# Optimization experiments

Measured on AMD Instinct MI355X. Metric: run time of the kernel, lower is better.

The kernel has to match this reference:

```python
import jax, jax.numpy as jnp
import numpy as np

NEG_SLOPE = 0.2   # PyG GATConv default leaky_relu slope
BN_EPS = 1e-5
SM_EPS = 1e-16    # PyG segment-softmax denominator epsilon


def gat_conv(x, src, dst, W, a_src, a_dst, bias, heads, out_ch, concat):
    # x: [N, F_in]; src/dst: [E] (self-loops already included)
    N = x.shape[0]
    h = (x @ W).reshape(N, heads, out_ch)              # [N, H, C]
    s = jnp.sum(h * a_src, axis=-1)                    # [N, H] per-node source score
    d = jnp.sum(h * a_dst, axis=-1)                    # [N, H] per-node dest score
    e = jax.nn.leaky_relu(s[src] + d[dst], NEG_SLOPE)  # [E, H]
    # segment softmax over edges grouped by destination node
    m = jax.ops.segment_max(e, dst, num_segments=N)
    m = jnp.where(jnp.isfinite(m), m, 0.0)
    p = jnp.exp(e - m[dst])                            # [E, H]
    denom = jax.ops.segment_sum(p, dst, num_segments=N)
    alpha = p / (denom[dst] + SM_EPS)                  # [E, H]
    # attention-weighted scatter-sum aggregation
    out = jax.ops.segment_sum(h[src] * alpha[:, :, None], dst, num_segments=N)  # [N, H, C]
    if concat:
        out = out.reshape(N, heads * out_ch)
    else:
        out = out.mean(axis=1)
    return out + bias


def setup_inputs() -> dict:
    key = jax.random.key(0)
    ks = jax.random.split(key, 12)
    N, E = 50000, 400000
    F_in, hidden, H1, H2, nclasses = 256, 64, 4, 1, 40
    x = jax.random.normal(ks[0], (N, F_in), dtype=jnp.float32)
    edge_index = jax.random.randint(ks[1], (2, E), 0, N, dtype=jnp.int64)
    g = 1.0 / np.sqrt(F_in)
    W1 = jax.random.normal(ks[2], (F_in, H1 * hidden), dtype=jnp.float32) * g
    a_src1 = jax.random.normal(ks[3], (H1, hidden), dtype=jnp.float32) * 0.1
    a_dst1 = jax.random.normal(ks[4], (H1, hidden), dtype=jnp.float32) * 0.1
    b1 = jnp.zeros((H1 * hidden,), dtype=jnp.float32)
    gamma = jnp.ones((H1 * hidden,), dtype=jnp.float32)
    beta = jnp.zeros((H1 * hidden,), dtype=jnp.float32)
    g2 = 1.0 / np.sqrt(H1 * hidden)
    W2 = jax.random.normal(ks[5], (H1 * hidden, H2 * nclasses), dtype=jnp.float32) * g2
    a_src2 = jax.random.normal(ks[6], (H2, nclasses), dtype=jnp.float32) * 0.1
    a_dst2 = jax.random.normal(ks[7], (H2, nclasses), dtype=jnp.float32) * 0.1
    b2 = jnp.zeros((nclasses,), dtype=jnp.float32)
    return {"x": x, "edge_index": edge_index, "W1": W1, "a_src1": a_src1,
            "a_dst1": a_dst1, "b1": b1, "gamma": gamma, "beta": beta,
            "W2": W2, "a_src2": a_src2, "a_dst2": a_dst2, "b2": b2}


def reference(x, edge_index, W1, a_src1, a_dst1, b1, gamma, beta, W2, a_src2, a_dst2, b2):
    N = x.shape[0]
    loop = jnp.arange(N, dtype=edge_index.dtype)
    src = jnp.concatenate([edge_index[0], loop])   # add self-loops (GATConv default)
    dst = jnp.concatenate([edge_index[1], loop])
    H1, hidden = a_src1.shape
    H2, nclasses = a_src2.shape
    h = gat_conv(x, src, dst, W1, a_src1, a_dst1, b1, H1, hidden, concat=True)
    # BatchNorm1d (training-mode batch statistics, biased variance)
    mu = h.mean(axis=0)
    var = h.var(axis=0)
    h = (h - mu) * jax.lax.rsqrt(var + BN_EPS) * gamma + beta
    h = jax.nn.elu(h)
    out = gat_conv(h, src, dst, W2, a_src2, a_dst2, b2, H2, nclasses, concat=False)
    return jax.nn.log_softmax(out, axis=-1)
```

## Files before the change

### kernel.cpp

```cpp
#include <hip/hip_runtime.h>
#include <hip/hip_fp16.h>

constexpr int FIN = 256;
constexpr int C1  = 256;
constexpr int HID = 64;
constexpr int H1N = 4;
constexpr int NC  = 40;
constexpr int CAP = 256;
constexpr int CAP2 = 128;

__global__ __launch_bounds__(64)
void detect_kernel(const int* __restrict__ ei, int* __restrict__ flag, int E)
{
    int lane = threadIdx.x;
    int q = lane * (E / 64);
    int v = ei[2 * q + 1];
    unsigned long long nz = __ballot(v != 0);
    if (lane == 0) flag[0] = (nz == 0ull) ? 2 : 1;
}

__global__ __launch_bounds__(256)
void init_kernel(int* __restrict__ counts, int* __restrict__ fill,
                 float* __restrict__ colsum, float* __restrict__ colsq, int N)
{
    int t = blockIdx.x * 256 + threadIdx.x;
    if (t < N) { counts[t] = 1; fill[t] = 0; }
    if (t < C1) { colsum[t] = 0.f; colsq[t] = 0.f; }
}

__global__ __launch_bounds__(256)
void gemm1_kernel(const float* __restrict__ X, const float* __restrict__ W,
                  const float* __restrict__ as1, const float* __restrict__ ad1,
                  __half* __restrict__ Hm, float* __restrict__ s1,
                  float* __restrict__ d1, int N)
{
    __shared__ float As[16][68];
    __shared__ float Bs[16][68];
    const int t    = threadIdx.x;
    const int tx   = t & 15;
    const int ty   = t >> 4;
    const int bm   = blockIdx.x * 64;
    const int head = blockIdx.y;
    const int bn   = head * 64;

    const int lrow = t >> 2;
    const int lk   = (t & 3) * 4;
    const int brow = t >> 4;
    const int bcol = (t & 15) * 4;

    float acc[4][4] = {};

    for (int k0 = 0; k0 < FIN; k0 += 16) {
        int ar = bm + lrow; if (ar > N - 1) ar = N - 1;
        float4 av = *(const float4*)(X + (size_t)ar * FIN + k0 + lk);
        float4 bv = *(const float4*)(W + (size_t)(k0 + brow) * C1 + bn + bcol);
        As[lk + 0][lrow] = av.x;
        As[lk + 1][lrow] = av.y;
        As[lk + 2][lrow] = av.z;
        As[lk + 3][lrow] = av.w;
        *(float4*)&Bs[brow][bcol] = bv;
        __syncthreads();
        #pragma unroll
        for (int kk = 0; kk < 16; ++kk) {
            float4 a = *(const float4*)&As[kk][ty * 4];
            float4 b = *(const float4*)&Bs[kk][tx * 4];
            float a4[4] = {a.x, a.y, a.z, a.w};
            float b4[4] = {b.x, b.y, b.z, b.w};
            #pragma unroll
            for (int i = 0; i < 4; ++i)
                #pragma unroll
                for (int j = 0; j < 4; ++j)
                    acc[i][j] += a4[i] * b4[j];
        }
        __syncthreads();
    }

    float sp[4] = {0, 0, 0, 0}, dp[4] = {0, 0, 0, 0};
    #pragma unroll
    for (int i = 0; i < 4; ++i) {
        int row = bm + ty * 4 + i;
        if (row < N) {
            __half2 p01 = __floats2half2_rn(acc[i][0], acc[i][1]);
            __half2 p23 = __floats2half2_rn(acc[i][2], acc[i][3]);
            uint2 pk;
            pk.x = *(unsigned int*)&p01;
            pk.y = *(unsigned int*)&p23;
            *(uint2*)(Hm + (size_t)row * C1 + bn + tx * 4) = pk;
            #pragma unroll
            for (int j = 0; j < 4; ++j) {
                int col = tx * 4 + j;
                float v = acc[i][j];
                sp[i] += v * as1[bn + col];
                dp[i] += v * ad1[bn + col];
            }
        }
    }
    #pragma unroll
    for (int off = 1; off < 16; off <<= 1) {
        #pragma unroll
        for (int i = 0; i < 4; ++i) {
            sp[i] += __shfl_xor(sp[i], off);
            dp[i] += __shfl_xor(dp[i], off);
        }
    }
    if (tx == 0) {
        #pragma unroll
        for (int i = 0; i < 4; ++i) {
            int row = bm + ty * 4 + i;
            if (row < N) {
                s1[row * H1N + head] = sp[i];
                d1[row * H1N + head] = dp[i];
            }
        }
    }
}

__global__ __launch_bounds__(256)
void hist_kernel(const int* __restrict__ ei, const int* __restrict__ flag,
                 int* __restrict__ counts, int E)
{
    int t = blockIdx.x * 256 + threadIdx.x;
    int stride = flag[0];
    if (t < E) atomicAdd(&counts[ei[(size_t)stride * (E + t)]], 1);
}

__global__ __launch_bounds__(1024)
void scan_kernel(const int* __restrict__ cnt, int* __restrict__ offs, int N)
{
    __shared__ int wsum[16];
    __shared__ int carry_s;
    const int t = threadIdx.x, lane = t & 63, w = t >> 6;
    if (t == 0) carry_s = 0;
    __syncthreads();
    for (int base = 0; base < N; base += 1024) {
        int idx = base + t;
        int v = (idx < N) ? cnt[idx] : 0;
        int incl = v;
        #pragma unroll
        for (int off = 1; off < 64; off <<= 1) {
            int u = __shfl_up(incl, off);
            if (lane >= off) incl += u;
        }
        if (lane == 63) wsum[w] = incl;
        __syncthreads();
        int wpre = 0;
        for (int i = 0; i < w; ++i) wpre += wsum[i];
        int c = carry_s;
        if (idx < N) offs[idx] = c + wpre + incl - v;
        __syncthreads();
        if (t == 1023) carry_s = c + wpre + incl;
        __syncthreads();
    }
    if (t == 0) offs[N] = carry_s;
}

__global__ __launch_bounds__(256)
void scatter_kernel(const int* __restrict__ ei, const int* __restrict__ flag,
                    const int* __restrict__ offs, int* __restrict__ fill,
                    int* __restrict__ ssrc, int E, int N)
{
    int t = blockIdx.x * 256 + threadIdx.x;
    if (t >= E + N) return;
    int stride = flag[0];
    int s, d;
    if (t < E) {
        s = ei[(size_t)stride * t];
        d = ei[(size_t)stride * (E + t)];
    } else {
        s = t - E; d = s;
    }
    int pos = offs[d] + atomicAdd(&fill[d], 1);
    ssrc[pos] = s;
}

__global__ __launch_bounds__(256)
void agg1_kernel(const __half* __restrict__ Hm, const float* __restrict__ s1,
                 const float* __restrict__ d1, const int* __restrict__ offs,
                 const int* __restrict__ ssrc, const float* __restrict__ b1,
                 float* __restrict__ out1, int N)
{
    __shared__ float alpha[H1N][CAP];
    __shared__ int   srcs[CAP];
    __shared__ float invs[H1N];
    const int n    = blockIdx.x;
    const int t    = threadIdx.x;
    const int lane = t & 63;
    const int w    = t >> 6;
    const int beg  = offs[n], end = offs[n + 1];
    const int deg  = end - beg;
    const float dh = d1[n * H1N + w];

    if (deg <= CAP) {
        float mloc = -1e30f;
        for (int i = lane; i < deg; i += 64) {
            int s = ssrc[beg + i];
            if (w == 0) srcs[i] = s;
            float e = s1[s * H1N + w] + dh;
            e = e > 0.f ? e : 0.2f * e;
            alpha[w][i] = e;
            mloc = fmaxf(mloc, e);
        }
        #pragma unroll
        for (int off = 32; off; off >>= 1) mloc = fmaxf(mloc, __shfl_xor(mloc, off));
        float ssum = 0.f;
        for (int i = lane; i < deg; i += 64) {
            float ex = __expf(alpha[w][i] - mloc);
            alpha[w][i] = ex;
            ssum += ex;
        }
        #pragma unroll
        for (int off = 32; off; off >>= 1) ssum += __shfl_xor(ssum, off);
        if (lane == 0) invs[w] = 1.f / (ssum + 1e-16f);
        __syncthreads();

        float acc0 = 0.f, acc1 = 0.f, acc2 = 0.f, acc3 = 0.f;
        int i = 0;
        for (; i + 4 <= deg; i += 4) {
            int s0 = srcs[i],     s1i = srcs[i + 1];
            int s2 = srcs[i + 2], s3i = srcs[i + 3];
            float a0 = alpha[w][i],     a1 = alpha[w][i + 1];
            float a2 = alpha[w][i + 2], a3 = alpha[w][i + 3];
            float v0 = __half2float(Hm[(size_t)s0  * C1 + t]);
            float v1 = __half2float(Hm[(size_t)s1i * C1 + t]);
            float v2 = __half2float(Hm[(size_t)s2  * C1 + t]);
            float v3 = __half2float(Hm[(size_t)s3i * C1 + t]);
            acc0 += v0 * a0; acc1 += v1 * a1;
            acc2 += v2 * a2; acc3 += v3 * a3;
        }
        for (; i < deg; ++i)
            acc0 += __half2float(Hm[(size_t)srcs[i] * C1 + t]) * alpha[w][i];
        float acc = (acc0 + acc1) + (acc2 + acc3);
        out1[(size_t)n * C1 + t] = acc * invs[w] + b1[t];
        return;
    }

    float mloc = -1e30f;
    for (int p = beg + lane; p < end; p += 64) {
        float e = s1[ssrc[p] * H1N + w] + dh;
        e = e > 0.f ? e : 0.2f * e;
        mloc = fmaxf(mloc, e);
    }
    #pragma unroll
    for (int off = 32; off; off >>= 1) mloc = fmaxf(mloc, __shfl_xor(mloc, off));
    float ssum = 0.f;
    for (int p = beg + lane; p < end; p += 64) {
        float e = s1[ssrc[p] * H1N + w] + dh;
        e = e > 0.f ? e : 0.2f * e;
        ssum += __expf(e - mloc);
    }
    #pragma unroll
    for (int off = 32; off; off >>= 1) ssum += __shfl_xor(ssum, off);
    if (lane == 0) invs[w] = 1.f / (ssum + 1e-16f);

    float acc0 = 0.f, acc1 = 0.f, acc2 = 0.f, acc3 = 0.f;
    for (int c0 = 0; c0 < deg; c0 += CAP) {
        int cnt = min(CAP, deg - c0);
        for (int i = lane; i < cnt; i += 64) {
            int p = beg + c0 + i;
            int s = ssrc[p];
            if (w == 0) srcs[i] = s;
            float e = s1[s * H1N + w] + dh;
            e = e > 0.f ? e : 0.2f * e;
            alpha[w][i] = __expf(e - mloc);
        }
        __syncthreads();
        int i = 0;
        for (; i + 4 <= cnt; i += 4) {
            int s0 = srcs[i],     s1i = srcs[i + 1];
            int s2 = srcs[i + 2], s3i = srcs[i + 3];
            float a0 = alpha[w][i],     a1 = alpha[w][i + 1];
            float a2 = alpha[w][i + 2], a3 = alpha[w][i + 3];
            float v0 = __half2float(Hm[(size_t)s0  * C1 + t]);
            float v1 = __half2float(Hm[(size_t)s1i * C1 + t]);
            float v2 = __half2float(Hm[(size_t)s2  * C1 + t]);
            float v3 = __half2float(Hm[(size_t)s3i * C1 + t]);
            acc0 += v0 * a0; acc1 += v1 * a1;
            acc2 += v2 * a2; acc3 += v3 * a3;
        }
        for (; i < cnt; ++i)
            acc0 += __half2float(Hm[(size_t)srcs[i] * C1 + t]) * alpha[w][i];
        __syncthreads();
    }
    float acc = (acc0 + acc1) + (acc2 + acc3);
    out1[(size_t)n * C1 + t] = acc * invs[w] + b1[t];
}

__global__ __launch_bounds__(256)
void bnstats_kernel(const float* __restrict__ out1, float* __restrict__ colsum,
                    float* __restrict__ colsq, int N)
{
    int t = threadIdx.x;
    float s = 0.f, q = 0.f;
    for (int r = blockIdx.x; r < N; r += gridDim.x) {
        float v = out1[(size_t)r * C1 + t];
        s += v; q += v * v;
    }
    atomicAdd(&colsum[t], s);
    atomicAdd(&colsq[t], q);
}

__global__ __launch_bounds__(256)
void bnfin_kernel(const float* __restrict__ colsum, const float* __restrict__ colsq,
                  const float* __restrict__ gamma, const float* __restrict__ beta,
                  float* __restrict__ scale, float* __restrict__ shift, int N)
{
    int t = threadIdx.x;
    float mu  = colsum[t] / (float)N;
    float var = colsq[t] / (float)N - mu * mu;
    float sc  = gamma[t] * rsqrtf(var + 1e-5f);
    scale[t] = sc;
    shift[t] = beta[t] - mu * sc;
}

__global__ __launch_bounds__(256)
void gemm2_kernel(const float* __restrict__ out1, const float* __restrict__ scale,
                  const float* __restrict__ shift, const float* __restrict__ W2,
                  const float* __restrict__ as2, const float* __restrict__ ad2,
                  float* __restrict__ h2, float* __restrict__ s2,
                  float* __restrict__ d2, int N)
{
    __shared__ float Asm[64][68];
    __shared__ float Wsm[64 * 48];
    const int t   = threadIdx.x;
    const int r   = t >> 2;
    const int jg  = t & 3;
    const int rb  = blockIdx.x * 64;
    const int row = rb + r;
    const int j0  = jg * 10;

    float acc[10] = {};

    for (int kc = 0; kc < C1; kc += 64) {
        #pragma unroll
        for (int idx = t; idx < 64 * 16; idx += 256) {
            int ar = idx >> 4;
            int cg = (idx & 15) * 4;
            int arow = rb + ar;
            float4 v = make_float4(0.f, 0.f, 0.f, 0.f);
            if (arow < N) {
                v = *(const float4*)(out1 + (size_t)arow * C1 + kc + cg);
                float4 sc = *(const float4*)(scale + kc + cg);
                float4 sh = *(const float4*)(shift + kc + cg);
                v.x = v.x * sc.x + sh.x;
                v.y = v.y * sc.y + sh.y;
                v.z = v.z * sc.z + sh.z;
                v.w = v.w * sc.w + sh.w;
                v.x = v.x > 0.f ? v.x : (__expf(v.x) - 1.f);
                v.y = v.y > 0.f ? v.y : (__expf(v.y) - 1.f);
                v.z = v.z > 0.f ? v.z : (__expf(v.z) - 1.f);
                v.w = v.w > 0.f ? v.w : (__expf(v.w) - 1.f);
            }
            *(float4*)&Asm[ar][cg] = v;
        }
        #pragma unroll
        for (int idx = t; idx < 64 * 40; idx += 256) {
            int k = idx / 40, j = idx - k * 40;
            Wsm[k * 48 + (j / 10) * 12 + (j % 10)] = W2[(size_t)(kc + k) * NC + j];
        }
        __syncthreads();
        #pragma unroll 4
        for (int k = 0; k < 64; ++k) {
            float a = Asm[r][k];
            const float* wp = &Wsm[k * 48 + jg * 12];
            float4 w0 = *(const float4*)(wp);
            float4 w1 = *(const float4*)(wp + 4);
            float2 wv = *(const float2*)(wp + 8);
            acc[0] += a * w0.x; acc[1] += a * w0.y;
            acc[2] += a * w0.z; acc[3] += a * w0.w;
            acc[4] += a * w1.x; acc[5] += a * w1.y;
            acc[6] += a * w1.z; acc[7] += a * w1.w;
            acc[8] += a * wv.x; acc[9] += a * wv.y;
        }
        __syncthreads();
    }

    float sp = 0.f, dp = 0.f;
    #pragma unroll
    for (int jj = 0; jj < 10; ++jj) {
        sp += acc[jj] * as2[j0 + jj];
        dp += acc[jj] * ad2[j0 + jj];
    }
    sp += __shfl_xor(sp, 1); sp += __shfl_xor(sp, 2);
    dp += __shfl_xor(dp, 1); dp += __shfl_xor(dp, 2);
    if (row < N) {
        if (jg == 0) { s2[row] = sp; d2[row] = dp; }
        #pragma unroll
        for (int jj = 0; jj < 10; jj += 2)
            *(float2*)(h2 + (size_t)row * NC + j0 + jj) =
                make_float2(acc[jj], acc[jj + 1]);
    }
}

__global__ __launch_bounds__(256)
void agg2_kernel(const float* __restrict__ h2, const float* __restrict__ s2,
                 const float* __restrict__ d2, const int* __restrict__ offs,
                 const int* __restrict__ ssrc, const float* __restrict__ b2,
                 float* __restrict__ out, int N)
{
    __shared__ float al[4][CAP2];
    __shared__ int   sr[4][CAP2];
    int w = threadIdx.x >> 6;
    int node = blockIdx.x * 4 + w;
    if (node >= N) return;
    int lane = threadIdx.x & 63;
    int beg = offs[node], end = offs[node + 1];
    int deg = end - beg;
    float dn = d2[node];

    float v;
    if (deg <= CAP2) {
        float mloc = -1e30f;
        for (int i = lane; i < deg; i += 64) {
            int s = ssrc[beg + i];
            sr[w][i] = s;
            float e = s2[s] + dn;
            e = e > 0.f ? e : 0.2f * e;
            al[w][i] = e;
            mloc = fmaxf(mloc, e);
        }
        #pragma unroll
        for (int off = 32; off; off >>= 1) mloc = fmaxf(mloc, __shfl_xor(mloc, off));
        float ssum = 0.f;
        for (int i = lane; i < deg; i += 64) {
            float ex = __expf(al[w][i] - mloc);
            al[w][i] = ex;
            ssum += ex;
        }
        #pragma unroll
        for (int off = 32; off; off >>= 1) ssum += __shfl_xor(ssum, off);
        float inv = 1.f / (ssum + 1e-16f);

        int j = lane < NC ? lane : 0;
        float acc0 = 0.f, acc1 = 0.f, acc2 = 0.f, acc3 = 0.f;
        int i = 0;
        for (; i + 4 <= deg; i += 4) {
            float a0 = al[w][i],     a1 = al[w][i + 1];
            float a2 = al[w][i + 2], a3 = al[w][i + 3];
            acc0 += h2[(size_t)sr[w][i]     * NC + j] * a0;
            acc1 += h2[(size_t)sr[w][i + 1] * NC + j] * a1;
            acc2 += h2[(size_t)sr[w][i + 2] * NC + j] * a2;
            acc3 += h2[(size_t)sr[w][i + 3] * NC + j] * a3;
        }
        for (; i < deg; ++i)
            acc0 += h2[(size_t)sr[w][i] * NC + j] * al[w][i];
        v = ((acc0 + acc1) + (acc2 + acc3)) * inv + b2[j];
    } else {
        float m = -1e30f, denom = 0.f;
        for (int p = beg; p < end; ++p) {
            float e = s2[ssrc[p]] + dn;
            e = e > 0.f ? e : 0.2f * e;
            float mn = fmaxf(m, e);
            denom = denom * __expf(m - mn) + __expf(e - mn);
            m = mn;
        }
        float inv = 1.f / (denom + 1e-16f);
        int j = lane < NC ? lane : 0;
        float acc = 0.f;
        for (int p = beg; p < end; ++p) {
            int s = ssrc[p];
            float e = s2[s] + dn;
            e = e > 0.f ? e : 0.2f * e;
            acc += h2[(size_t)s * NC + j] * (__expf(e - m) * inv);
        }
        v = acc + b2[j];
    }

    float vm = lane < NC ? v : -1e30f;
    #pragma unroll
    for (int off = 32; off > 0; off >>= 1) vm = fmaxf(vm, __shfl_xor(vm, off));
    float ex = lane < NC ? __expf(v - vm) : 0.f;
    #pragma unroll
    for (int off = 32; off > 0; off >>= 1) ex += __shfl_xor(ex, off);
    if (lane < NC) out[(size_t)node * NC + lane] = v - vm - __logf(ex);
}

extern "C" void kernel_launch(void* const* d_in, const int* in_sizes, int n_in,
                              void* d_out, int out_size, void* d_ws, size_t ws_size,
                              hipStream_t stream)
{
    const float* x   = (const float*)d_in[0];
    const int*   ei  = (const int*)d_in[1];
    const float* W1  = (const float*)d_in[2];
    const float* as1 = (const float*)d_in[3];
    const float* ad1 = (const float*)d_in[4];
    const float* b1  = (const float*)d_in[5];
    const float* gm  = (const float*)d_in[6];
    const float* bt  = (const float*)d_in[7];
    const float* W2  = (const float*)d_in[8];
    const float* as2 = (const float*)d_in[9];
    const float* ad2 = (const float*)d_in[10];
    const float* b2  = (const float*)d_in[11];
    const int N = in_sizes[0] / FIN;
    const int E = in_sizes[1] / 2;

    char* p = (char*)d_ws;
    auto take = [&](size_t bytes) {
        char* r = p; p += (bytes + 255) & ~(size_t)255; return r;
    };
    __half* Hm    = (__half*)take((size_t)N * C1 * 2);
    float* out1   = (float*)take((size_t)N * C1 * 4);
    float* h2     = (float*)take((size_t)N * NC * 4);
    float* s1     = (float*)take((size_t)N * H1N * 4);
    float* d1     = (float*)take((size_t)N * H1N * 4);
    float* s2     = (float*)take((size_t)N * 4);
    float* d2v    = (float*)take((size_t)N * 4);
    float* colsum = (float*)take(C1 * 4);
    float* colsq  = (float*)take(C1 * 4);
    float* bnsc   = (float*)take(C1 * 4);
    float* bnsh   = (float*)take(C1 * 4);
    int*   counts = (int*)take((size_t)N * 4);
    int*   offs   = (int*)take((size_t)(N + 1) * 4);
    int*   fill   = (int*)take((size_t)N * 4);
    int*   ssrc   = (int*)take((size_t)(E + N) * 4);
    int*   eflag  = (int*)take(256);

    detect_kernel<<<1, 64, 0, stream>>>(ei, eflag, E);
    init_kernel<<<(N + 255) / 256, 256, 0, stream>>>(counts, fill, colsum, colsq, N);
    gemm1_kernel<<<dim3((N + 63) / 64, H1N), 256, 0, stream>>>(x, W1, as1, ad1, Hm, s1, d1, N);
    hist_kernel<<<(E + 255) / 256, 256, 0, stream>>>(ei, eflag, counts, E);
    scan_kernel<<<1, 1024, 0, stream>>>(counts, offs, N);
    scatter_kernel<<<(E + N + 255) / 256, 256, 0, stream>>>(ei, eflag, offs, fill, ssrc, E, N);
    agg1_kernel<<<N, 256, 0, stream>>>(Hm, s1, d1, offs, ssrc, b1, out1, N);
    bnstats_kernel<<<1024, 256, 0, stream>>>(out1, colsum, colsq, N);
    bnfin_kernel<<<1, 256, 0, stream>>>(colsum, colsq, gm, bt, bnsc, bnsh, N);
    gemm2_kernel<<<(N + 63) / 64, 256, 0, stream>>>(out1, bnsc, bnsh, W2, as2, ad2, h2, s2, d2v, N);
    agg2_kernel<<<(N + 3) / 4, 256, 0, stream>>>(h2, s2, d2v, offs, ssrc, b2, (float*)d_out, N);
}
```

Measured before the change: 495.1 us.

## Replace FP32 SIMT first-layer GEMM with FP16 MFMA using pre-cast inputs

Adds kernels that cast X to padded fp16 and transpose-cast W1 to fp16. The first-layer GEMM is replaced with one built on 16x16x32 fp16 MFMA instructions, reading operands straight from global memory with no LDS staging, and the per-head attention score reductions are fused into its epilogue. This targets the FP32 FMA cost of the N x 256 x 256 GEMM. In exchange it adds an extra pass over X, lowers input precision to fp16, and writes Hm with scattered 2-byte stores.

```diff
diff --git a/kernel.cpp b/kernel.cpp
--- a/kernel.cpp
+++ b/kernel.cpp
@@ -9,6 +9,9 @@
 constexpr int CAP = 256;
 constexpr int CAP2 = 128;
 
+using f16x8 = __attribute__((ext_vector_type(8))) _Float16;
+using f32x4 = __attribute__((ext_vector_type(4))) float;
+
 __global__ __launch_bounds__(64)
 void detect_kernel(const int* __restrict__ ei, int* __restrict__ flag, int E)
 {
@@ -29,88 +32,97 @@
 }
 
 __global__ __launch_bounds__(256)
-void gemm1_kernel(const float* __restrict__ X, const float* __restrict__ W,
-                  const float* __restrict__ as1, const float* __restrict__ ad1,
-                  __half* __restrict__ Hm, float* __restrict__ s1,
-                  float* __restrict__ d1, int N)
-{
-    __shared__ float As[16][68];
-    __shared__ float Bs[16][68];
+void xcast_kernel(const float* __restrict__ X, _Float16* __restrict__ Xh,
+                  int N, int NPAD)
+{
+    int idx = (blockIdx.x * 256 + threadIdx.x) * 4;
+    if (idx >= NPAD * FIN) return;
+    int row = idx >> 8;
+    _Float16 h4[4];
+    if (row < N) {
+        float4 v = *(const float4*)(X + idx);
+        h4[0] = (_Float16)v.x; h4[1] = (_Float16)v.y;
+        h4[2] = (_Float16)v.z; h4[3] = (_Float16)v.w;
+    } else {
+        h4[0] = h4[1] = h4[2] = h4[3] = (_Float16)0.f;
+    }
+    *(uint2*)(Xh + idx) = *(uint2*)h4;
+}
+
+__global__ __launch_bounds__(256)
+void w1cast_kernel(const float* __restrict__ W1, _Float16* __restrict__ W1t)
+{
+    __shared__ float tile[64][65];
+    int bx = blockIdx.x & 3, by = blockIdx.x >> 2;
+    int t = threadIdx.x;
+    int c = t & 63, r4 = (t >> 6) * 16;
+    #pragma unroll
+    for (int i = 0; i < 16; ++i)
+        tile[r4 + i][c] = W1[(size_t)(by * 64 + r4 + i) * C1 + bx * 64 + c];
+    __syncthreads();
+    #pragma unroll
+    for (int i = 0; i < 16; ++i)
+        W1t[(size_t)(bx * 64 + r4 + i) * FIN + by * 64 + c] =
+            (_Float16)tile[c][r4 + i];
+}
+
+__global__ __launch_bounds__(256)
+void gemm1_mfma_kernel(const _Float16* __restrict__ Xh,
+                       const _Float16* __restrict__ W1t,
+                       const float* __restrict__ as1, const float* __restrict__ ad1,
+                       __half* __restrict__ Hm, float* __restrict__ s1,
+                       float* __restrict__ d1, int N)
+{
     const int t    = threadIdx.x;
-    const int tx   = t & 15;
-    const int ty   = t >> 4;
-    const int bm   = blockIdx.x * 64;
-    const int head = blockIdx.y;
-    const int bn   = head * 64;
-
-    const int lrow = t >> 2;
-    const int lk   = (t & 3) * 4;
-    const int brow = t >> 4;
-    const int bcol = (t & 15) * 4;
-
-    float acc[4][4] = {};
-
-    for (int k0 = 0; k0 < FIN; k0 += 16) {
-        int ar = bm + lrow; if (ar > N - 1) ar = N - 1;
-        float4 av = *(const float4*)(X + (size_t)ar * FIN + k0 + lk);
-        float4 bv = *(const float4*)(W + (size_t)(k0 + brow) * C1 + bn + bcol);
-        As[lk + 0][lrow] = av.x;
-        As[lk + 1][lrow] = av.y;
-        As[lk + 2][lrow] = av.z;
-        As[lk + 3][lrow] = av.w;
-        *(float4*)&Bs[brow][bcol] = bv;
-        __syncthreads();
-        #pragma unroll
-        for (int kk = 0; kk < 16; ++kk) {
-            float4 a = *(const float4*)&As[kk][ty * 4];
-            float4 b = *(const float4*)&Bs[kk][tx * 4];
-            float a4[4] = {a.x, a.y, a.z, a.w};
-            float b4[4] = {b.x, b.y, b.z, b.w};
+    const int lane = t & 63;
+    const int w    = t >> 6;
+    const int rowbase = blockIdx.x * 64 + w * 16;
+    const int lrow = lane & 15;
+    const int kgrp = lane >> 4;
+    const int arow = rowbase + lrow;
+
+    f32x4 acc[16];
+    #pragma unroll
+    for (int i = 0; i < 16; ++i) acc[i] = f32x4{0.f, 0.f, 0.f, 0.f};
+
+    #pragma unroll
+    for (int ks = 0; ks < 8; ++ks) {
+        f16x8 a = *(const f16x8*)(Xh + (size_t)arow * FIN + ks * 32 + kgrp * 8);
+        #pragma unroll
+        for (int ct = 0; ct < 16; ++ct) {
+            f16x8 b = *(const f16x8*)(W1t + (size_t)(ct * 16 + lrow) * FIN
+                                      + ks * 32 + kgrp * 8);
+            acc[ct] = __builtin_amdgcn_mfma_f32_16x16x32_f16(a, b, acc[ct], 0, 0, 0);
+        }
+    }
+
+    #pragma unroll
+    for (int reg = 0; reg < 4; ++reg) {
+        int r = rowbase + kgrp * 4 + reg;
+        bool ok = r < N;
+        #pragma unroll
+        for (int h = 0; h < 4; ++h) {
+            float sp = 0.f, dp = 0.f;
             #pragma unroll
-            for (int i = 0; i < 4; ++i)
-                #pragma unroll
-                for (int j = 0; j < 4; ++j)
-                    acc[i][j] += a4[i] * b4[j];
-        }
-        __syncthreads();
-    }
-
-    float sp[4] = {0, 0, 0, 0}, dp[4] = {0, 0, 0, 0};
-    #pragma unroll
-    for (int i = 0; i < 4; ++i) {
-        int row = bm + ty * 4 + i;
-        if (row < N) {
-            __half2 p01 = __floats2half2_rn(acc[i][0], acc[i][1]);
-            __half2 p23 = __floats2half2_rn(acc[i][2], acc[i][3]);
-            uint2 pk;
-            pk.x = *(unsigned int*)&p01;
-            pk.y = *(unsigned int*)&p23;
-            *(uint2*)(Hm + (size_t)row * C1 + bn + tx * 4) = pk;
+            for (int q = 0; q < 4; ++q) {
+                int ct = h * 4 + q;
+                float v = acc[ct][reg];
+                sp += v * as1[ct * 16 + lrow];
+                dp += v * ad1[ct * 16 + lrow];
+            }
+            sp += __shfl_xor(sp, 1); sp += __shfl_xor(sp, 2);
+            sp += __shfl_xor(sp, 4); sp += __shfl_xor(sp, 8);
+            dp += __shfl_xor(dp, 1); dp += __shfl_xor(dp, 2);
+            dp += __shfl_xor(dp, 4); dp += __shfl_xor(dp, 8);
+            if (ok && lrow == 0) {
+                s1[r * H1N + h] = sp;
+                d1[r * H1N + h] = dp;
+            }
+        }
+        if (ok) {
             #pragma unroll
-            for (int j = 0; j < 4; ++j) {
-                int col = tx * 4 + j;
-                float v = acc[i][j];
-                sp[i] += v * as1[bn + col];
-                dp[i] += v * ad1[bn + col];
-            }
-        }
-    }
-    #pragma unroll
-    for (int off = 1; off < 16; off <<= 1) {
-        #pragma unroll
-        for (int i = 0; i < 4; ++i) {
-            sp[i] += __shfl_xor(sp[i], off);
-            dp[i] += __shfl_xor(dp[i], off);
-        }
-    }
-    if (tx == 0) {
-        #pragma unroll
-        for (int i = 0; i < 4; ++i) {
-            int row = bm + ty * 4 + i;
-            if (row < N) {
-                s1[row * H1N + head] = sp[i];
-                d1[row * H1N + head] = dp[i];
-            }
+            for (int ct = 0; ct < 16; ++ct)
+                Hm[(size_t)r * C1 + ct * 16 + lrow] = __float2half(acc[ct][reg]);
         }
     }
 }
@@ -492,12 +504,15 @@
     const float* b2  = (const float*)d_in[11];
     const int N = in_sizes[0] / FIN;
     const int E = in_sizes[1] / 2;
+    const int NPAD = (N + 63) & ~63;
 
     char* p = (char*)d_ws;
     auto take = [&](size_t bytes) {
         char* r = p; p += (bytes + 255) & ~(size_t)255; return r;
     };
-    __half* Hm    = (__half*)take((size_t)N * C1 * 2);
+    __half* Hm       = (__half*)take((size_t)N * C1 * 2);
+    _Float16* Xh     = (_Float16*)take((size_t)NPAD * FIN * 2);
+    _Float16* W1t    = (_Float16*)take((size_t)FIN * C1 * 2);
     float* out1   = (float*)take((size_t)N * C1 * 4);
     float* h2     = (float*)take((size_t)N * NC * 4);
     float* s1     = (float*)take((size_t)N * H1N * 4);
@@ -516,7 +531,9 @@
 
     detect_kernel<<<1, 64, 0, stream>>>(ei, eflag, E);
     init_kernel<<<(N + 255) / 256, 256, 0, stream>>>(counts, fill, colsum, colsq, N);
-    gemm1_kernel<<<dim3((N + 63) / 64, H1N), 256, 0, stream>>>(x, W1, as1, ad1, Hm, s1, d1, N);
+    xcast_kernel<<<(NPAD * FIN / 4 + 255) / 256, 256, 0, stream>>>(x, Xh, N, NPAD);
+    w1cast_kernel<<<16, 256, 0, stream>>>(W1, W1t);
+    gemm1_mfma_kernel<<<NPAD / 64, 256, 0, stream>>>(Xh, W1t, as1, ad1, Hm, s1, d1, N);
     hist_kernel<<<(E + 255) / 256, 256, 0, stream>>>(ei, eflag, counts, E);
     scan_kernel<<<1, 1024, 0, stream>>>(counts, offs, N);
     scatter_kernel<<<(E + N + 255) / 256, 256, 0, stream>>>(ei, eflag, offs, fill, ssrc, E, N);
```

Result: faster. 483.5 us (-2.3%).
